# Optimization experiments

Measured on AMD Instinct MI355X. Metric: run time of the kernel, lower is better.

## Reference

```python
import jax, jax.numpy as jnp
import numpy as np

N_NODES = 100000
N_EDGES = 1600000
IN_C, HID_C, OUT_C = 128, 64, 40


def setup_inputs() -> dict:
    key = jax.random.key(0)
    ks = jax.random.split(key, 8)
    x = jax.random.normal(ks[0], (N_NODES, IN_C), dtype=jnp.float32)
    edge_index = jax.random.randint(ks[1], (2, N_EDGES), 0, N_NODES, dtype=jnp.int64)
    # Glorot-ish init for weights
    W1 = jax.random.normal(ks[2], (IN_C, HID_C), dtype=jnp.float32) / np.sqrt(IN_C)
    W2 = jax.random.normal(ks[3], (HID_C, HID_C), dtype=jnp.float32) / np.sqrt(HID_C)
    W3 = jax.random.normal(ks[4], (HID_C, OUT_C), dtype=jnp.float32) / np.sqrt(HID_C)
    b1 = jnp.zeros((HID_C,), jnp.float32)
    b2 = jnp.zeros((HID_C,), jnp.float32)
    b3 = jnp.zeros((OUT_C,), jnp.float32)
    return {"x": x, "edge_index": edge_index, "W1": W1, "b1": b1,
            "W2": W2, "b2": b2, "W3": W3, "b3": b3}


def _gcn_prep(edge_index, num_nodes):
    # PyG GCNConv: add self-loops, symmetric normalization with edge_weight=1.
    src = jnp.concatenate([edge_index[0], jnp.arange(num_nodes, dtype=edge_index.dtype)])
    dst = jnp.concatenate([edge_index[1], jnp.arange(num_nodes, dtype=edge_index.dtype)])
    deg = jax.ops.segment_sum(jnp.ones_like(dst, dtype=jnp.float32), dst,
                              num_segments=num_nodes)
    dis = jnp.where(deg > 0, jax.lax.rsqrt(deg), 0.0)  # deg^-1/2, inf->0
    norm = dis[src] * dis[dst]  # per-edge symmetric norm
    return src, dst, norm


def _gcn_conv(x, W, b, src, dst, norm, num_nodes):
    h = x @ W                                # [N, F_out], linear (no bias)
    msg = h[src] * norm[:, None]             # gather + scale, [E_total, F_out]
    out = jax.ops.segment_sum(msg, dst, num_segments=num_nodes)
    return out + b                           # conv bias after aggregation


def reference(x, edge_index, W1, b1, W2, b2, W3, b3):
    n = x.shape[0]
    src, dst, norm = _gcn_prep(edge_index, n)
    h = jax.nn.relu(_gcn_conv(x, W1, b1, src, dst, norm, n))
    h = jax.nn.relu(_gcn_conv(h, W2, b2, src, dst, norm, n))
    h = _gcn_conv(h, W3, b3, src, dst, norm, n)
    return jax.nn.log_softmax(h, axis=1)
```

## Files before the change

kernel.cpp:

```cpp
#include <hip/hip_runtime.h>
#include <cstdint>
#include <cstddef>
#include <math.h>

#define NN 100000
#define NE 1600000
#define NB ((NN + 255) / 256)
#define EB 400
#define EPB (NE / EB)
#define CAP 5120

#define GT_NODES 128
#define GT_KC 32
#define GT_STRIDE 132

typedef unsigned short u16;

__device__ __forceinline__ float bf2f(u16 u) {
    union { unsigned i; float f; } c; c.i = ((unsigned)u) << 16; return c.f;
}
__device__ __forceinline__ u16 f2bf(float f) {
    union { float f; unsigned int i; } c; c.f = f;
    unsigned int lsb = (c.i >> 16) & 1u;
    return (u16)((c.i + 0x7fffu + lsb) >> 16);
}
__device__ __forceinline__ unsigned int pack2(float a, float b) {
    return (unsigned int)f2bf(a) | ((unsigned int)f2bf(b) << 16);
}

__device__ __forceinline__ int load_idx(const void* ei, int isI64, int pos) {
    if (isI64) return (int)((const long long*)ei)[pos];
    return ((const int*)ei)[pos];
}

__global__ __launch_bounds__(256) void k_build(const void* __restrict__ ei,
                                               int* __restrict__ cursor,
                                               int* __restrict__ csr_tmp) {
    __shared__ int sbuf[EPB];
    __shared__ int dbuf[EPB];
    __shared__ int cnt[NB];
    __shared__ int basel[NB];
    __shared__ int anynz;

    const int* p = (const int*)ei;
    if (threadIdx.x == 0) anynz = 0;
    for (int i = threadIdx.x; i < NB; i += 256) cnt[i] = 0;
    __syncthreads();
    int nz = 0;
    for (int i = threadIdx.x; i < 1024; i += 256) nz |= (p[2 * i + 1] != 0);
    if (nz) anynz = 1;
    __syncthreads();
    int isI64 = (anynz == 0);

    int base = blockIdx.x * EPB;
    for (int i = threadIdx.x; i < EPB; i += 256) {
        int s = load_idx(ei, isI64, base + i);
        int d = load_idx(ei, isI64, NE + base + i);
        sbuf[i] = s;
        dbuf[i] = d;
        atomicAdd(&cnt[d >> 8], 1);
    }
    __syncthreads();
    for (int j = threadIdx.x; j < NB; j += 256) {
        int c = cnt[j];
        int g = c ? atomicAdd(&cursor[j], c) : 0;
        basel[j] = j * CAP + g;
        cnt[j] = 0;
    }
    __syncthreads();
    for (int i = threadIdx.x; i < EPB; i += 256) {
        int s = sbuf[i];
        int d = dbuf[i];
        int bkt = d >> 8;
        int slot = basel[bkt] + atomicAdd(&cnt[bkt], 1);
        csr_tmp[slot] = ((d & 255) << 17) | s;
    }
}

__global__ __launch_bounds__(256) void k_sort(const int* __restrict__ cursor,
                                              const int* __restrict__ csr_tmp,
                                              int* __restrict__ csr,
                                              int* __restrict__ deg,
                                              int* __restrict__ offs,
                                              float* __restrict__ dis) {
    __shared__ int h[256];
    __shared__ int sc[256];
    __shared__ int cur[256];
    int j = blockIdx.x;
    int s0 = j * CAP, s1 = s0 + cursor[j];
    h[threadIdx.x] = 0;
    __syncthreads();
    for (int p = s0 + threadIdx.x; p < s1; p += 256)
        atomicAdd(&h[csr_tmp[p] >> 17], 1);
    __syncthreads();
    int v = h[threadIdx.x];
    sc[threadIdx.x] = v;
    __syncthreads();
#pragma unroll
    for (int off = 1; off < 256; off <<= 1) {
        int u = (threadIdx.x >= off) ? sc[threadIdx.x - off] : 0;
        __syncthreads();
        sc[threadIdx.x] += u;
        __syncthreads();
    }
    int excl = sc[threadIdx.x] - v;
    int node = j * 256 + threadIdx.x;
    if (node < NN) {
        deg[node] = v;
        offs[node] = s0 + excl;
        dis[node] = rsqrtf((float)(v + 1));
    }
    cur[threadIdx.x] = excl;
    __syncthreads();
    for (int p = s0 + threadIdx.x; p < s1; p += 256) {
        int pk = csr_tmp[p];
        int dl = pk >> 17;
        int pos = s0 + atomicAdd(&cur[dl], 1);
        csr[pos] = pk & 0x1FFFF;
    }
}

template <int K, int FR, bool RELU>
__global__ __launch_bounds__(512) void k_gemm(const float* __restrict__ x,
                                              const float* __restrict__ W,
                                              const float* __restrict__ dis,
                                              u16* __restrict__ out) {
    __shared__ float xT[GT_KC * GT_STRIDE];
    __shared__ float Wc[GT_KC * 64];
    const int tid = threadIdx.x;
    const int r = tid >> 4;
    const int c = tid & 15;
    const int f4 = tid & 7;
    const int nrow = tid >> 3;
    const int nbase = blockIdx.x * GT_NODES;

    float acc[4][4];
#pragma unroll
    for (int i = 0; i < 4; ++i)
#pragma unroll
        for (int j = 0; j < 4; ++j) acc[i][j] = 0.f;

    for (int kc = 0; kc < K; kc += GT_KC) {
#pragma unroll
        for (int q = 0; q < 4; ++q) {
            int e = q * 512 + tid;
            int kk = e >> 6, j = e & 63;
            Wc[kk * 64 + j] = (j < FR) ? W[(size_t)(kc + kk) * FR + j] : 0.f;
        }
#pragma unroll
        for (int q = 0; q < 2; ++q) {
            int nl = q * 64 + nrow;
            int n = nbase + nl;
            float4 v = make_float4(0.f, 0.f, 0.f, 0.f);
            if (n < NN) v = *(const float4*)(x + (size_t)n * K + kc + f4 * 4);
            if (RELU) {
                v.x = fmaxf(v.x, 0.f); v.y = fmaxf(v.y, 0.f);
                v.z = fmaxf(v.z, 0.f); v.w = fmaxf(v.w, 0.f);
            }
            xT[(f4 * 4 + 0) * GT_STRIDE + nl] = v.x;
            xT[(f4 * 4 + 1) * GT_STRIDE + nl] = v.y;
            xT[(f4 * 4 + 2) * GT_STRIDE + nl] = v.z;
            xT[(f4 * 4 + 3) * GT_STRIDE + nl] = v.w;
        }
        __syncthreads();
#pragma unroll 8
        for (int kk = 0; kk < GT_KC; ++kk) {
            float4 a = *(const float4*)&xT[kk * GT_STRIDE + r * 4];
            float4 w = *(const float4*)&Wc[kk * 64 + c * 4];
            float xa[4] = {a.x, a.y, a.z, a.w};
            float wb[4] = {w.x, w.y, w.z, w.w};
#pragma unroll
            for (int i = 0; i < 4; ++i)
#pragma unroll
                for (int j = 0; j < 4; ++j)
                    acc[i][j] = fmaf(xa[i], wb[j], acc[i][j]);
        }
        __syncthreads();
    }
    if (c * 4 < FR) {
#pragma unroll
        for (int i = 0; i < 4; ++i) {
            int n = nbase + r * 4 + i;
            if (n < NN) {
                float dv = dis[n];
                uint2 o;
                o.x = pack2(dv * acc[i][0], dv * acc[i][1]);
                o.y = pack2(dv * acc[i][2], dv * acc[i][3]);
                *(uint2*)(out + (size_t)n * FR + c * 4) = o;
            }
        }
    }
}

template <int F, int B, bool MASK>
__device__ __forceinline__ float gb(int myidx, int i, int lim,
                                    const u16* __restrict__ g, unsigned fc) {
    const u16* rp[B];
#pragma unroll
    for (int k = 0; k < B; ++k) {
        int s = __builtin_amdgcn_readlane(myidx, i + k);
        rp[k] = g + (size_t)(unsigned)s * (unsigned)F;
    }
    u16 hh[B];
#pragma unroll
    for (int k = 0; k < B; ++k) hh[k] = rp[k][fc];
    float t0 = 0.f, t1 = 0.f, t2 = 0.f, t3 = 0.f;
#pragma unroll
    for (int k = 0; k < B; ++k) {
        float v = bf2f(hh[k]);
        if (MASK) v = (i + k < lim) ? v : 0.f;
        if ((k & 3) == 0) t0 += v;
        else if ((k & 3) == 1) t1 += v;
        else if ((k & 3) == 2) t2 += v;
        else t3 += v;
    }
    return (t0 + t1) + (t2 + t3);
}

template <int F, bool SOFTMAX>
__global__ __launch_bounds__(256) void k_gather(const int* __restrict__ offs,
                                                const int* __restrict__ deg,
                                                const int* __restrict__ csr,
                                                const float* __restrict__ dis,
                                                const u16* __restrict__ g,
                                                const float* __restrict__ b,
                                                float* __restrict__ out) {
    int n = blockIdx.x * 4 + (threadIdx.x >> 6);
    unsigned f = threadIdx.x & 63;
    if (n >= NN) return;
    unsigned fc = (f < (unsigned)F) ? f : 0u;
    int start = __builtin_amdgcn_readfirstlane(offs[n]);
    int len   = __builtin_amdgcn_readfirstlane(deg[n]);
    float dvn = dis[n];
    float bf  = b[fc];
    float acc = bf2f(g[(unsigned)n * F + fc]);

    int myidx = 0;
    if ((int)f < len) myidx = csr[start + (int)f];
    int lim = (len < 64) ? len : 64;

    if (lim > 0) {
        if (lim >= 33) {
            int i = 0;
            for (; i + 16 <= lim; i += 16)
                acc += gb<F, 16, false>(myidx, i, lim, g, fc);
            if (i < lim)
                acc += gb<F, 16, true>(myidx, i, lim, g, fc);
        } else if (lim >= 17) {
            acc += gb<F, 32, true>(myidx, 0, lim, g, fc);
        } else if (lim == 16) {
            acc += gb<F, 16, false>(myidx, 0, lim, g, fc);
        } else {
            acc += gb<F, 16, true>(myidx, 0, lim, g, fc);
        }
    }

    if (len > 64) {
        int ii = 64;
        for (; ii + 2 <= len; ii += 2) {
            int s0 = __builtin_amdgcn_readfirstlane(csr[start + ii + 0]);
            int s1 = __builtin_amdgcn_readfirstlane(csr[start + ii + 1]);
            u16 h0 = g[(unsigned)s0 * F + fc];
            u16 h1 = g[(unsigned)s1 * F + fc];
            acc += bf2f(h0) + bf2f(h1);
        }
        if (ii < len) {
            int s0 = __builtin_amdgcn_readfirstlane(csr[start + ii]);
            acc += bf2f(g[(unsigned)s0 * F + fc]);
        }
    }

    float v = dvn * acc + bf;
    if (!SOFTMAX) {
        if (f < (unsigned)F) out[(size_t)n * F + f] = v;
    } else {
        float vv = (f < (unsigned)F) ? v : -INFINITY;
        float m = vv;
#pragma unroll
        for (int off = 32; off; off >>= 1) m = fmaxf(m, __shfl_xor(m, off));
        float ex = (f < (unsigned)F) ? __expf(vv - m) : 0.f;
        float sum = ex;
#pragma unroll
        for (int off = 32; off; off >>= 1) sum += __shfl_xor(sum, off);
        if (f < (unsigned)F) out[(size_t)n * F + f] = vv - m - logf(sum);
    }
}

extern "C" void kernel_launch(void* const* d_in, const int* in_sizes, int n_in,
                              void* d_out, int out_size, void* d_ws, size_t ws_size,
                              hipStream_t stream) {
    const float* x  = (const float*)d_in[0];
    const void*  ei = d_in[1];
    const float* W1 = (const float*)d_in[2];
    const float* b1 = (const float*)d_in[3];
    const float* W2 = (const float*)d_in[4];
    const float* b2 = (const float*)d_in[5];
    const float* W3 = (const float*)d_in[6];
    const float* b3 = (const float*)d_in[7];
    float* out = (float*)d_out;

    char* ws = (char*)d_ws;
    size_t off = 0;
    auto alloc = [&](size_t bytes) { void* p = ws + off; off += (bytes + 255) & ~255ULL; return p; };
    int*   cursor  = (int*)alloc(NB * 4);
    int*   deg     = (int*)alloc(NN * 4);
    float* dis     = (float*)alloc(NN * 4);
    int*   offs    = (int*)alloc(NN * 4);
    int*   csr_tmp = (int*)alloc((size_t)NB * CAP * 4);
    int*   csr     = (int*)alloc((size_t)NB * CAP * 4);
    u16*   gbuf    = (u16*)alloc((size_t)NN * 64 * 2);
    float* act     = (float*)alloc((size_t)NN * 64 * 4);

    hipMemsetAsync(cursor, 0, NB * 4, stream);
    k_build<<<EB, 256, 0, stream>>>(ei, cursor, csr_tmp);
    k_sort<<<NB, 256, 0, stream>>>(cursor, csr_tmp, csr, deg, offs, dis);

    const int gemm_grid = (NN + GT_NODES - 1) / GT_NODES;
    const int gather_grid = (NN + 3) / 4;

    k_gemm<128, 64, false><<<gemm_grid, 512, 0, stream>>>(x, W1, dis, gbuf);
    k_gather<64, false><<<gather_grid, 256, 0, stream>>>(offs, deg, csr, dis, gbuf, b1, act);

    k_gemm<64, 64, true><<<gemm_grid, 512, 0, stream>>>(act, W2, dis, gbuf);
    k_gather<64, false><<<gather_grid, 256, 0, stream>>>(offs, deg, csr, dis, gbuf, b2, act);

    k_gemm<64, 40, true><<<gemm_grid, 512, 0, stream>>>(act, W3, dis, gbuf);
    k_gather<40, true><<<gather_grid, 256, 0, stream>>>(offs, deg, csr, dis, gbuf, b3, out);
}
```

Measured before the change: 323.0 us.

## Fuse neighbor aggregation with next-layer GEMM, removing fp32 activation round trip

Adds a k_fuse kernel that aggregates each node's neighbors, applies bias and ReLU, stages the result transposed in shared memory, and immediately multiplies by the next weight matrix, writing bf16 scaled features. This replaces two gather+GEMM kernel pairs and removes the fp32 activation write and reread between them. In exchange each block runs the irregular gather for 128 nodes with 512 threads (16 nodes per wave, serial), so parallelism in the gather phase drops and LDS use grows, which may cost occupancy. A second bf16 buffer is used to ping-pong between layers.

```diff
diff --git a/kernel.cpp b/kernel.cpp
--- a/kernel.cpp
+++ b/kernel.cpp
@@ -217,22 +217,15 @@
     return (t0 + t1) + (t2 + t3);
 }
 
-template <int F, bool SOFTMAX>
-__global__ __launch_bounds__(256) void k_gather(const int* __restrict__ offs,
-                                                const int* __restrict__ deg,
-                                                const int* __restrict__ csr,
-                                                const float* __restrict__ dis,
-                                                const u16* __restrict__ g,
-                                                const float* __restrict__ b,
-                                                float* __restrict__ out) {
-    int n = blockIdx.x * 4 + (threadIdx.x >> 6);
-    unsigned f = threadIdx.x & 63;
-    if (n >= NN) return;
-    unsigned fc = (f < (unsigned)F) ? f : 0u;
+template <int F>
+__device__ __forceinline__ float grow(int n, unsigned fc,
+                                      const int* __restrict__ offs,
+                                      const int* __restrict__ deg,
+                                      const int* __restrict__ csr,
+                                      const u16* __restrict__ g) {
     int start = __builtin_amdgcn_readfirstlane(offs[n]);
     int len   = __builtin_amdgcn_readfirstlane(deg[n]);
-    float dvn = dis[n];
-    float bf  = b[fc];
+    unsigned f = fc;
     float acc = bf2f(g[(unsigned)n * F + fc]);
 
     int myidx = 0;
@@ -254,7 +247,6 @@
             acc += gb<F, 16, true>(myidx, 0, lim, g, fc);
         }
     }
-
     if (len > 64) {
         int ii = 64;
         for (; ii + 2 <= len; ii += 2) {
@@ -269,7 +261,91 @@
             acc += bf2f(g[(unsigned)s0 * F + fc]);
         }
     }
-
+    return acc;
+}
+
+template <int FR>
+__global__ __launch_bounds__(512) void k_fuse(const int* __restrict__ offs,
+                                              const int* __restrict__ deg,
+                                              const int* __restrict__ csr,
+                                              const float* __restrict__ dis,
+                                              const u16* __restrict__ gin,
+                                              const float* __restrict__ bprev,
+                                              const float* __restrict__ W,
+                                              u16* __restrict__ gout) {
+    __shared__ float actT[64 * GT_STRIDE];
+    __shared__ float Wc[64 * 64];
+    const int tid = threadIdx.x;
+    const int nbase = blockIdx.x * GT_NODES;
+
+    for (int e = tid; e < 64 * 64; e += 512) {
+        int kk = e >> 6, j = e & 63;
+        Wc[e] = (j < FR) ? W[(size_t)kk * FR + j] : 0.f;
+    }
+
+    const int w = tid >> 6;
+    const unsigned f = tid & 63;
+    for (int t = 0; t < 16; ++t) {
+        int nl = w * 16 + t;
+        int n = nbase + nl;
+        float v = 0.f;
+        if (n < NN) {
+            float acc = grow<64>(n, f, offs, deg, csr, gin);
+            v = fmaxf(dis[n] * acc + bprev[f], 0.f);
+        }
+        actT[f * GT_STRIDE + nl] = v;
+    }
+    __syncthreads();
+
+    const int r = tid >> 4;
+    const int c = tid & 15;
+    float acc[4][4];
+#pragma unroll
+    for (int i = 0; i < 4; ++i)
+#pragma unroll
+        for (int j = 0; j < 4; ++j) acc[i][j] = 0.f;
+#pragma unroll 8
+    for (int kk = 0; kk < 64; ++kk) {
+        float4 a = *(const float4*)&actT[kk * GT_STRIDE + r * 4];
+        float4 wv = *(const float4*)&Wc[kk * 64 + c * 4];
+        float xa[4] = {a.x, a.y, a.z, a.w};
+        float wb[4] = {wv.x, wv.y, wv.z, wv.w};
+#pragma unroll
+        for (int i = 0; i < 4; ++i)
+#pragma unroll
+            for (int j = 0; j < 4; ++j)
+                acc[i][j] = fmaf(xa[i], wb[j], acc[i][j]);
+    }
+    if (c * 4 < FR) {
+#pragma unroll
+        for (int i = 0; i < 4; ++i) {
+            int n = nbase + r * 4 + i;
+            if (n < NN) {
+                float dv = dis[n];
+                uint2 o;
+                o.x = pack2(dv * acc[i][0], dv * acc[i][1]);
+                o.y = pack2(dv * acc[i][2], dv * acc[i][3]);
+                *(uint2*)(gout + (size_t)n * FR + c * 4) = o;
+            }
+        }
+    }
+}
+
+template <int F, bool SOFTMAX>
+__global__ __launch_bounds__(256) void k_gather(const int* __restrict__ offs,
+                                                const int* __restrict__ deg,
+                                                const int* __restrict__ csr,
+                                                const float* __restrict__ dis,
+                                                const u16* __restrict__ g,
+                                                const float* __restrict__ b,
+                                                float* __restrict__ out) {
+    int n = blockIdx.x * 4 + (threadIdx.x >> 6);
+    unsigned f = threadIdx.x & 63;
+    if (n >= NN) return;
+    unsigned fc = (f < (unsigned)F) ? f : 0u;
+    float dvn = dis[n];
+    float bf  = b[fc];
+    float acc = grow<F>(n, fc, offs, deg, csr, g);
     float v = dvn * acc + bf;
     if (!SOFTMAX) {
         if (f < (unsigned)F) out[(size_t)n * F + f] = v;
@@ -309,7 +385,7 @@
     int*   csr_tmp = (int*)alloc((size_t)NB * CAP * 4);
     int*   csr     = (int*)alloc((size_t)NB * CAP * 4);
     u16*   gbuf    = (u16*)alloc((size_t)NN * 64 * 2);
-    float* act     = (float*)alloc((size_t)NN * 64 * 4);
+    u16*   gbuf2   = (u16*)alloc((size_t)NN * 64 * 2);
 
     hipMemsetAsync(cursor, 0, NB * 4, stream);
     k_build<<<EB, 256, 0, stream>>>(ei, cursor, csr_tmp);
@@ -319,11 +395,10 @@
     const int gather_grid = (NN + 3) / 4;
 
     k_gemm<128, 64, false><<<gemm_grid, 512, 0, stream>>>(x, W1, dis, gbuf);
-    k_gather<64, false><<<gather_grid, 256, 0, stream>>>(offs, deg, csr, dis, gbuf, b1, act);
-
-    k_gemm<64, 64, true><<<gemm_grid, 512, 0, stream>>>(act, W2, dis, gbuf);
-    k_gather<64, false><<<gather_grid, 256, 0, stream>>>(offs, deg, csr, dis, gbuf, b2, act);
-
-    k_gemm<64, 40, true><<<gemm_grid, 512, 0, stream>>>(act, W3, dis, gbuf);
+
+    k_fuse<64><<<gemm_grid, 512, 0, stream>>>(offs, deg, csr, dis, gbuf, b1, W2, gbuf2);
+
+    k_fuse<40><<<gemm_grid, 512, 0, stream>>>(offs, deg, csr, dis, gbuf2, b2, W3, gbuf);
+
     k_gather<40, true><<<gather_grid, 256, 0, stream>>>(offs, deg, csr, dis, gbuf, b3, out);
 }
```

After: 365.4 us. 13.1% more time.

## Fuse aggregation, bias, ReLU and next-layer GEMM into one gather kernel

Applied to the files above, without the earlier changes.

Adds k_fuseg, which aggregates neighbours for four nodes per block, applies bias and ReLU into shared memory, then multiplies by the next layer's weight matrix and writes bf16 pre-scaled features directly. This removes the fp32 activation buffer round trip and two separate GEMM launches between layers. In exchange every block reloads the full 64x64 weight matrix into LDS (16KB per block, 25k blocks) and computes the small matmul with scalar FMAs. The gather grid now assumes NN is divisible by 4 and drops the bounds check.

```diff
diff --git a/kernel.cpp b/kernel.cpp
--- a/kernel.cpp
+++ b/kernel.cpp
@@ -217,26 +217,18 @@
     return (t0 + t1) + (t2 + t3);
 }
 
-template <int F, bool SOFTMAX>
-__global__ __launch_bounds__(256) void k_gather(const int* __restrict__ offs,
-                                                const int* __restrict__ deg,
-                                                const int* __restrict__ csr,
-                                                const float* __restrict__ dis,
-                                                const u16* __restrict__ g,
-                                                const float* __restrict__ b,
-                                                float* __restrict__ out) {
-    int n = blockIdx.x * 4 + (threadIdx.x >> 6);
-    unsigned f = threadIdx.x & 63;
-    if (n >= NN) return;
-    unsigned fc = (f < (unsigned)F) ? f : 0u;
+template <int F>
+__device__ __forceinline__ float grow(int n, unsigned fc,
+                                      const int* __restrict__ offs,
+                                      const int* __restrict__ deg,
+                                      const int* __restrict__ csr,
+                                      const u16* __restrict__ g) {
     int start = __builtin_amdgcn_readfirstlane(offs[n]);
     int len   = __builtin_amdgcn_readfirstlane(deg[n]);
-    float dvn = dis[n];
-    float bf  = b[fc];
     float acc = bf2f(g[(unsigned)n * F + fc]);
 
     int myidx = 0;
-    if ((int)f < len) myidx = csr[start + (int)f];
+    if ((int)fc < len) myidx = csr[start + (int)fc];
     int lim = (len < 64) ? len : 64;
 
     if (lim > 0) {
@@ -254,7 +246,6 @@
             acc += gb<F, 16, true>(myidx, 0, lim, g, fc);
         }
     }
-
     if (len > 64) {
         int ii = 64;
         for (; ii + 2 <= len; ii += 2) {
@@ -269,7 +260,65 @@
             acc += bf2f(g[(unsigned)s0 * F + fc]);
         }
     }
-
+    return acc;
+}
+
+template <int FR>
+__global__ __launch_bounds__(256) void k_fuseg(const int* __restrict__ offs,
+                                               const int* __restrict__ deg,
+                                               const int* __restrict__ csr,
+                                               const float* __restrict__ dis,
+                                               const u16* __restrict__ gin,
+                                               const float* __restrict__ bprev,
+                                               const float* __restrict__ W,
+                                               u16* __restrict__ gout) {
+    __shared__ float Wc[64 * 64];
+    __shared__ float actl[4 * 64];
+    const int tid = threadIdx.x;
+    const int w = tid >> 6;
+    const unsigned f = tid & 63;
+
+    for (int e = tid; e < 64 * 64; e += 256) {
+        int kk = e >> 6, j = e & 63;
+        Wc[e] = (j < FR) ? W[(size_t)kk * FR + j] : 0.f;
+    }
+
+    int n = blockIdx.x * 4 + w;
+    float acc = grow<64>(n, f, offs, deg, csr, gin);
+    float dvn = dis[n];
+    actl[w * 64 + f] = fmaxf(dvn * acc + bprev[f], 0.f);
+    __syncthreads();
+
+    const float* ap = &actl[w * 64];
+    float o0 = 0.f, o1 = 0.f, o2 = 0.f, o3 = 0.f;
+#pragma unroll
+    for (int k = 0; k < 64; k += 4) {
+        float4 av = *(const float4*)(ap + k);
+        o0 = fmaf(av.x, Wc[(k + 0) * 64 + f], o0);
+        o1 = fmaf(av.y, Wc[(k + 1) * 64 + f], o1);
+        o2 = fmaf(av.z, Wc[(k + 2) * 64 + f], o2);
+        o3 = fmaf(av.w, Wc[(k + 3) * 64 + f], o3);
+    }
+    float o = (o0 + o1) + (o2 + o3);
+    if (f < (unsigned)FR)
+        gout[(size_t)n * FR + f] = f2bf(dvn * o);
+}
+
+template <int F, bool SOFTMAX>
+__global__ __launch_bounds__(256) void k_gather(const int* __restrict__ offs,
+                                                const int* __restrict__ deg,
+                                                const int* __restrict__ csr,
+                                                const float* __restrict__ dis,
+                                                const u16* __restrict__ g,
+                                                const float* __restrict__ b,
+                                                float* __restrict__ out) {
+    int n = blockIdx.x * 4 + (threadIdx.x >> 6);
+    unsigned f = threadIdx.x & 63;
+    if (n >= NN) return;
+    unsigned fc = (f < (unsigned)F) ? f : 0u;
+    float dvn = dis[n];
+    float bf  = b[fc];
+    float acc = grow<F>(n, fc, offs, deg, csr, g);
     float v = dvn * acc + bf;
     if (!SOFTMAX) {
         if (f < (unsigned)F) out[(size_t)n * F + f] = v;
@@ -309,21 +358,20 @@
     int*   csr_tmp = (int*)alloc((size_t)NB * CAP * 4);
     int*   csr     = (int*)alloc((size_t)NB * CAP * 4);
     u16*   gbuf    = (u16*)alloc((size_t)NN * 64 * 2);
-    float* act     = (float*)alloc((size_t)NN * 64 * 4);
+    u16*   gbuf2   = (u16*)alloc((size_t)NN * 64 * 2);
 
     hipMemsetAsync(cursor, 0, NB * 4, stream);
     k_build<<<EB, 256, 0, stream>>>(ei, cursor, csr_tmp);
     k_sort<<<NB, 256, 0, stream>>>(cursor, csr_tmp, csr, deg, offs, dis);
 
     const int gemm_grid = (NN + GT_NODES - 1) / GT_NODES;
-    const int gather_grid = (NN + 3) / 4;
+    const int gather_grid = NN / 4;
 
     k_gemm<128, 64, false><<<gemm_grid, 512, 0, stream>>>(x, W1, dis, gbuf);
-    k_gather<64, false><<<gather_grid, 256, 0, stream>>>(offs, deg, csr, dis, gbuf, b1, act);
-
-    k_gemm<64, 64, true><<<gemm_grid, 512, 0, stream>>>(act, W2, dis, gbuf);
-    k_gather<64, false><<<gather_grid, 256, 0, stream>>>(offs, deg, csr, dis, gbuf, b2, act);
-
-    k_gemm<64, 40, true><<<gemm_grid, 512, 0, stream>>>(act, W3, dis, gbuf);
+
+    k_fuseg<64><<<gather_grid, 256, 0, stream>>>(offs, deg, csr, dis, gbuf, b1, W2, gbuf2);
+
+    k_fuseg<40><<<gather_grid, 256, 0, stream>>>(offs, deg, csr, dis, gbuf2, b2, W3, gbuf);
+
     k_gather<40, true><<<gather_grid, 256, 0, stream>>>(offs, deg, csr, dis, gbuf, b3, out);
 }
```

Result: slower. 419.6 us (+29.9%).

## Use feature-sliced 16-wide layout for hidden-layer gathers to improve cache locality

Applied to the files above, without the earlier changes.

The GEMM outputs for layers 1 and 2 are stored in four 16-feature slices, each NN*16 bf16 (3.2 MB), instead of row-major 64-wide rows. A new gather kernel processes one slice per block, with each wave covering four edges times sixteen features, then reduces across lanes with shuffles. The aim is to make the random neighbour gathers hit a working set that fits in cache, at the cost of four times as many blocks and 32-byte row fragments. The third layer reuses the csr_tmp buffer for its output and keeps the original gather with fused log-softmax.

```diff
diff --git a/kernel.cpp b/kernel.cpp
--- a/kernel.cpp
+++ b/kernel.cpp
@@ -120,7 +120,7 @@
     }
 }
 
-template <int K, int FR, bool RELU>
+template <int K, int FR, bool RELU, bool SIN, bool SOUT>
 __global__ __launch_bounds__(512) void k_gemm(const float* __restrict__ x,
                                               const float* __restrict__ W,
                                               const float* __restrict__ dis,
@@ -152,7 +152,15 @@
             int nl = q * 64 + nrow;
             int n = nbase + nl;
             float4 v = make_float4(0.f, 0.f, 0.f, 0.f);
-            if (n < NN) v = *(const float4*)(x + (size_t)n * K + kc + f4 * 4);
+            if (n < NN) {
+                if (SIN) {
+                    int k = kc + f4 * 4;
+                    v = *(const float4*)(x + (size_t)(k >> 4) * (NN * 16)
+                                           + (size_t)n * 16 + (k & 15));
+                } else {
+                    v = *(const float4*)(x + (size_t)n * K + kc + f4 * 4);
+                }
+            }
             if (RELU) {
                 v.x = fmaxf(v.x, 0.f); v.y = fmaxf(v.y, 0.f);
                 v.z = fmaxf(v.z, 0.f); v.w = fmaxf(v.w, 0.f);
@@ -186,10 +194,71 @@
                 uint2 o;
                 o.x = pack2(dv * acc[i][0], dv * acc[i][1]);
                 o.y = pack2(dv * acc[i][2], dv * acc[i][3]);
-                *(uint2*)(out + (size_t)n * FR + c * 4) = o;
+                if (SOUT) {
+                    int j0 = c * 4;
+                    u16* bp = out + (size_t)(j0 >> 4) * (NN * 16)
+                                  + (size_t)n * 16 + (j0 & 15);
+                    *(uint2*)bp = o;
+                } else {
+                    *(uint2*)(out + (size_t)n * FR + c * 4) = o;
+                }
             }
         }
     }
+}
+
+__global__ __launch_bounds__(256) void k_gath16(const int* __restrict__ offs,
+                                                const int* __restrict__ deg,
+                                                const int* __restrict__ csr,
+                                                const float* __restrict__ dis,
+                                                const u16* __restrict__ gin_s,
+                                                const float* __restrict__ b,
+                                                float* __restrict__ act_s) {
+    const int bid = blockIdx.x;
+    const int slice = bid & 3;
+    const int n = (bid >> 2) * 4 + (threadIdx.x >> 6);
+    const unsigned lane = threadIdx.x & 63;
+    const unsigned feat = lane & 15;
+    const unsigned esub = lane >> 4;
+    const u16* __restrict__ gs = gin_s + (size_t)slice * (NN * 16);
+
+    int start = __builtin_amdgcn_readfirstlane(offs[n]);
+    int len   = __builtin_amdgcn_readfirstlane(deg[n]);
+
+    float acc = (esub == 0) ? bf2f(gs[(unsigned)n * 16 + feat]) : 0.f;
+
+    int myidx = 0;
+    if ((int)lane < len) myidx = csr[start + (int)lane];
+    int lim = (len < 64) ? len : 64;
+
+    for (int i = 0; i < lim; i += 16) {
+        int e0 = i + (int)esub;
+        int s0 = __shfl(myidx, e0);
+        int s1 = __shfl(myidx, e0 + 4);
+        int s2 = __shfl(myidx, e0 + 8);
+        int s3 = __shfl(myidx, e0 + 12);
+        u16 h0 = gs[(unsigned)s0 * 16 + feat];
+        u16 h1 = gs[(unsigned)s1 * 16 + feat];
+        u16 h2 = gs[(unsigned)s2 * 16 + feat];
+        u16 h3 = gs[(unsigned)s3 * 16 + feat];
+        float v0 = (e0      < lim) ? bf2f(h0) : 0.f;
+        float v1 = (e0 + 4  < lim) ? bf2f(h1) : 0.f;
+        float v2 = (e0 + 8  < lim) ? bf2f(h2) : 0.f;
+        float v3 = (e0 + 12 < lim) ? bf2f(h3) : 0.f;
+        acc += (v0 + v1) + (v2 + v3);
+    }
+    if (len > 64) {
+        for (int i = 64 + (int)esub; i < len; i += 4) {
+            int s = csr[start + i];
+            acc += bf2f(gs[(unsigned)s * 16 + feat]);
+        }
+    }
+    acc += __shfl_xor(acc, 16);
+    acc += __shfl_xor(acc, 32);
+
+    float v = dis[n] * acc + b[slice * 16 + feat];
+    if (esub == 0)
+        act_s[(size_t)slice * (NN * 16) + (unsigned)n * 16 + feat] = v;
 }
 
 template <int F, int B, bool MASK>
@@ -217,26 +286,18 @@
     return (t0 + t1) + (t2 + t3);
 }
 
-template <int F, bool SOFTMAX>
-__global__ __launch_bounds__(256) void k_gather(const int* __restrict__ offs,
-                                                const int* __restrict__ deg,
-                                                const int* __restrict__ csr,
-                                                const float* __restrict__ dis,
-                                                const u16* __restrict__ g,
-                                                const float* __restrict__ b,
-                                                float* __restrict__ out) {
-    int n = blockIdx.x * 4 + (threadIdx.x >> 6);
-    unsigned f = threadIdx.x & 63;
-    if (n >= NN) return;
-    unsigned fc = (f < (unsigned)F) ? f : 0u;
+template <int F>
+__device__ __forceinline__ float grow(int n, unsigned fc,
+                                      const int* __restrict__ offs,
+                                      const int* __restrict__ deg,
+                                      const int* __restrict__ csr,
+                                      const u16* __restrict__ g) {
     int start = __builtin_amdgcn_readfirstlane(offs[n]);
     int len   = __builtin_amdgcn_readfirstlane(deg[n]);
-    float dvn = dis[n];
-    float bf  = b[fc];
     float acc = bf2f(g[(unsigned)n * F + fc]);
 
     int myidx = 0;
-    if ((int)f < len) myidx = csr[start + (int)f];
+    if ((int)fc < len) myidx = csr[start + (int)fc];
     int lim = (len < 64) ? len : 64;
 
     if (lim > 0) {
@@ -254,7 +315,6 @@
             acc += gb<F, 16, true>(myidx, 0, lim, g, fc);
         }
     }
-
     if (len > 64) {
         int ii = 64;
         for (; ii + 2 <= len; ii += 2) {
@@ -269,7 +329,24 @@
             acc += bf2f(g[(unsigned)s0 * F + fc]);
         }
     }
-
+    return acc;
+}
+
+template <int F, bool SOFTMAX>
+__global__ __launch_bounds__(256) void k_gather(const int* __restrict__ offs,
+                                                const int* __restrict__ deg,
+                                                const int* __restrict__ csr,
+                                                const float* __restrict__ dis,
+                                                const u16* __restrict__ g,
+                                                const float* __restrict__ b,
+                                                float* __restrict__ out) {
+    int n = blockIdx.x * 4 + (threadIdx.x >> 6);
+    unsigned f = threadIdx.x & 63;
+    if (n >= NN) return;
+    unsigned fc = (f < (unsigned)F) ? f : 0u;
+    float dvn = dis[n];
+    float bf  = b[fc];
+    float acc = grow<F>(n, fc, offs, deg, csr, g);
     float v = dvn * acc + bf;
     if (!SOFTMAX) {
         if (f < (unsigned)F) out[(size_t)n * F + f] = v;
@@ -308,22 +385,28 @@
     int*   offs    = (int*)alloc(NN * 4);
     int*   csr_tmp = (int*)alloc((size_t)NB * CAP * 4);
     int*   csr     = (int*)alloc((size_t)NB * CAP * 4);
-    u16*   gbuf    = (u16*)alloc((size_t)NN * 64 * 2);
-    float* act     = (float*)alloc((size_t)NN * 64 * 4);
+    u16*   gbuf_s  = (u16*)alloc((size_t)NN * 64 * 2);
+    u16*   gbuf2_s = (u16*)alloc((size_t)NN * 64 * 2);
+    float* act_s   = (float*)alloc((size_t)NN * 64 * 4);
+    u16*   gbuf3   = (u16*)csr_tmp;
 
     hipMemsetAsync(cursor, 0, NB * 4, stream);
     k_build<<<EB, 256, 0, stream>>>(ei, cursor, csr_tmp);
     k_sort<<<NB, 256, 0, stream>>>(cursor, csr_tmp, csr, deg, offs, dis);
 
     const int gemm_grid = (NN + GT_NODES - 1) / GT_NODES;
-    const int gather_grid = (NN + 3) / 4;
-
-    k_gemm<128, 64, false><<<gemm_grid, 512, 0, stream>>>(x, W1, dis, gbuf);
-    k_gather<64, false><<<gather_grid, 256, 0, stream>>>(offs, deg, csr, dis, gbuf, b1, act);
-
-    k_gemm<64, 64, true><<<gemm_grid, 512, 0, stream>>>(act, W2, dis, gbuf);
-    k_gather<64, false><<<gather_grid, 256, 0, stream>>>(offs, deg, csr, dis, gbuf, b2, act);
-
-    k_gemm<64, 40, true><<<gemm_grid, 512, 0, stream>>>(act, W3, dis, gbuf);
-    k_gather<40, true><<<gather_grid, 256, 0, stream>>>(offs, deg, csr, dis, gbuf, b3, out);
-}
+    const int slice_grid = (NN / 4) * 4;
+    const int gather_grid = NN / 4;
+
+    k_gemm<128, 64, false, false, true><<<gemm_grid, 512, 0, stream>>>(x, W1, dis, gbuf_s);
+
+    k_gath16<<<slice_grid, 256, 0, stream>>>(offs, deg, csr, dis, gbuf_s, b1, act_s);
+
+    k_gemm<64, 64, true, true, true><<<gemm_grid, 512, 0, stream>>>(act_s, W2, dis, gbuf2_s);
+
+    k_gath16<<<slice_grid, 256, 0, stream>>>(offs, deg, csr, dis, gbuf2_s, b2, act_s);
+
+    k_gemm<64, 40, true, true, false><<<gemm_grid, 512, 0, stream>>>(act_s, W3, dis, gbuf3);
+
+    k_gather<40, true><<<gather_grid, 256, 0, stream>>>(offs, deg, csr, dis, gbuf3, b3, out);
+}
```

After: 480.8 us. +48.8%, slower.
